# Optimization experiments

Hardware: AMD Instinct MI355X
Metric: run time of the kernel (lower is better)

## Reference

```python
import jax, jax.numpy as jnp
from jax import lax
import numpy as np

B, C, H, W = 4, 256, 64, 64
CQK = C // 8  # 32


def conv3x3(x, w, b):
    # x: [B,C_in,H,W], w: [C_out,C_in,3,3], b: [C_out]
    y = lax.conv_general_dilated(x, w, window_strides=(1, 1), padding='SAME',
                                 dimension_numbers=('NCHW', 'OIHW', 'NCHW'))
    return y + b[None, :, None, None]


def setup_inputs() -> dict:
    key = jax.random.key(0)
    ks = jax.random.split(key, 8)
    scale = 0.02
    return {
        'x': jax.random.normal(ks[0], (B, C, H, W), dtype=jnp.float32),
        'wq': jax.random.normal(ks[1], (CQK, C, 3, 3), dtype=jnp.float32) * scale,
        'bq': jax.random.normal(ks[2], (CQK,), dtype=jnp.float32) * scale,
        'wk': jax.random.normal(ks[3], (CQK, C, 3, 3), dtype=jnp.float32) * scale,
        'bk': jax.random.normal(ks[4], (CQK,), dtype=jnp.float32) * scale,
        'wv': jax.random.normal(ks[5], (C, C, 3, 3), dtype=jnp.float32) * scale,
        'bv': jax.random.normal(ks[6], (C,), dtype=jnp.float32) * scale,
        'gamma': jax.random.normal(ks[7], (1,), dtype=jnp.float32) * scale,
    }


def reference(x, wq, bq, wk, bk, wv, bv, gamma):
    b, c, h, w = x.shape
    n = h * w
    # Q: [B, N, C//8]  (permute(0,2,1) of the flattened conv output)
    q = conv3x3(x, wq, bq).reshape(b, -1, n).transpose(0, 2, 1)
    # K: [B, C//8, N]
    k = conv3x3(x, wk, bk).reshape(b, -1, n)
    # s: [B, N_q, N_k]
    s = jnp.einsum('bqd,bdk->bqk', q, k)
    # NOTE: original uses Softmax(dim=-2), i.e. over the QUERY axis
    attn_T = jax.nn.softmax(s, axis=-2)
    # V: [B, C, N]
    v = conv3x3(x, wv, bv).reshape(b, c, n)
    # o = bmm(V, attn_T): [B, C, N]
    o = jnp.einsum('bcq,bqk->bck', v, attn_T).reshape(b, c, h, w)
    return x + gamma * o
```

## Files before the change

### kernel.cpp

```cpp
#include <hip/hip_runtime.h>
#include <cstddef>

#define N_PIX 4096
#define HW 64
#define LOG2E 1.4426950408889634f
#define SHIFT2 28.8539008177793f

typedef __attribute__((ext_vector_type(8))) short bf16x8;
typedef __attribute__((ext_vector_type(4))) float f32x4;
typedef unsigned int u32;

static __device__ __forceinline__ unsigned short f2bf(float f) {
    union { float f; unsigned u; } v; v.f = f;
    unsigned r = v.u + 0x7fffu + ((v.u >> 16) & 1u);
    return (unsigned short)(r >> 16);
}
static __device__ __forceinline__ float bf2f(unsigned short s) {
    union { unsigned u; float f; } v; v.u = (unsigned)s << 16;
    return v.f;
}
static __device__ __forceinline__ unsigned pack_bf16_trunc(float lo, float hi) {
    union { float f; unsigned u; } a, b; a.f = hi; b.f = lo;
    return __builtin_amdgcn_perm(a.u, b.u, 0x07060302u);
}
static __device__ __forceinline__ void gll16(const void* g, void* l) {
    __builtin_amdgcn_global_load_lds(
        (const __attribute__((address_space(1))) u32*)g,
        (__attribute__((address_space(3))) u32*)l, 16, 0, 0);
}

__global__ __launch_bounds__(256) void prep_kernel(
    const float* __restrict__ x, unsigned short* __restrict__ xbf,
    const float* __restrict__ wq, const float* __restrict__ wk,
    const float* __restrict__ wv, unsigned short* __restrict__ wAll,
    unsigned short* __restrict__ zp)
{
    const int tid = threadIdx.x;
    if (blockIdx.z < 4) {
        __shared__ unsigned short Ts[64][72];
        const int px0 = blockIdx.x * 64, ci0 = blockIdx.y * 64, b = blockIdx.z;
        const float* xb = x + ((size_t)b * 256 + ci0) * N_PIX;

#pragma unroll
        for (int r = 0; r < 4; ++r) {
            int c = r * 16 + (tid >> 4);
            int p4 = (tid & 15) * 4;
            float4 v = *(const float4*)&xb[(size_t)c * N_PIX + px0 + p4];
            Ts[c][p4 + 0] = f2bf(v.x);
            Ts[c][p4 + 1] = f2bf(v.y);
            Ts[c][p4 + 2] = f2bf(v.z);
            Ts[c][p4 + 3] = f2bf(v.w);
        }
        __syncthreads();
#pragma unroll
        for (int r = 0; r < 2; ++r) {
            int id = tid * 2 + r;
            int p = id >> 3, c8 = (id & 7) * 8;
            ushort4 lo, hi;
            lo.x = Ts[c8 + 0][p]; lo.y = Ts[c8 + 1][p];
            lo.z = Ts[c8 + 2][p]; lo.w = Ts[c8 + 3][p];
            hi.x = Ts[c8 + 4][p]; hi.y = Ts[c8 + 5][p];
            hi.z = Ts[c8 + 6][p]; hi.w = Ts[c8 + 7][p];
            size_t off = ((size_t)b * N_PIX + px0 + p) * 256 + ci0 + c8;
            *(ushort4*)&xbf[off]     = lo;
            *(ushort4*)&xbf[off + 4] = hi;
        }
    } else {
        const int f = blockIdx.y * 64 + blockIdx.x;
#pragma unroll
        for (int base = 0; base < 2; ++base) {
            int gid = base * 65536 + f * 256 + tid;
            if (gid < 256) zp[gid] = 0;
            if (gid >= 72 * 320 * 4) continue;
            int part = gid & 3;
            int m = (gid >> 2) % 320;
            int kb = gid / 1280;
            int t = kb >> 3;
            int ci0 = (kb & 7) * 32 + part * 8;
            const float* src; int co; float sc = 1.f;
            if (m < 256)      { src = wv; co = m; }
            else if (m < 288) { src = wq; co = m - 256; sc = LOG2E; }
            else              { src = wk; co = m - 288; }
            ushort4 lo, hi;
            lo.x = f2bf(sc * src[((size_t)co * 256 + ci0 + 0) * 9 + t]);
            lo.y = f2bf(sc * src[((size_t)co * 256 + ci0 + 1) * 9 + t]);
            lo.z = f2bf(sc * src[((size_t)co * 256 + ci0 + 2) * 9 + t]);
            lo.w = f2bf(sc * src[((size_t)co * 256 + ci0 + 3) * 9 + t]);
            hi.x = f2bf(sc * src[((size_t)co * 256 + ci0 + 4) * 9 + t]);
            hi.y = f2bf(sc * src[((size_t)co * 256 + ci0 + 5) * 9 + t]);
            hi.z = f2bf(sc * src[((size_t)co * 256 + ci0 + 6) * 9 + t]);
            hi.w = f2bf(sc * src[((size_t)co * 256 + ci0 + 7) * 9 + t]);
            size_t off = ((size_t)kb * 320 + m) * 32 + part * 8;
            *(ushort4*)&wAll[off]     = lo;
            *(ushort4*)&wAll[off + 4] = hi;
        }
    }
}

__global__ __launch_bounds__(256, 2) void conv_gemm_v7(
    const unsigned short* __restrict__ xbf, const unsigned short* __restrict__ wAll,
    const float* __restrict__ bq, const float* __restrict__ bk,
    const float* __restrict__ bv, const unsigned short* __restrict__ zpage,
    unsigned short* __restrict__ vbf, unsigned short* __restrict__ qt,
    unsigned short* __restrict__ kt)
{
    __shared__ unsigned short Bl[4 * 7168];

    const int tid = threadIdx.x;
    const int w = tid >> 6, lane = tid & 63, quad = lane >> 4, l15 = lane & 15;
    const int y = blockIdx.x, rh = blockIdx.y, b = blockIdx.z;
    const int rg = w >> 1;
    const int pxh = w & 1;

    const unsigned short* xb = xbf + (size_t)b * N_PIX * 256;
    const unsigned short* aSrc = wAll + (size_t)rh * 160 * 32;

    auto stage = [&](int kb, int buf) {
        const int t_ = kb >> 3;
        const int ty = t_ / 3;
        const int dy = ty - 1, dx = t_ - ty * 3 - 1;
        const int gy = y + dy;
        const bool rowOK = ((unsigned)gy < 64u);
        const int ci0 = (kb & 7) * 32;
        const unsigned short* aS = aSrc + (size_t)kb * 10240;
        unsigned short* tile = &Bl[buf * 7168];
#pragma unroll
        for (int r = 0; r < 4; ++r) {
            const int c = r * 4 + w;
            if (r == 3 && w >= 2) continue;
            if (c < 10) {
                int o = c * 1024 + lane * 16;
                int u = o ^ (((o >> 7) & 7) << 4);
                gll16(aS + (u >> 1), tile + c * 512);
            } else {
                int o = (c - 10) * 1024 + lane * 16;
                int u = o ^ (((o >> 7) & 7) << 4);
                int px = u >> 6, k16 = (u >> 4) & 3;
                int gx = px + dx;
                const unsigned short* src =
                    (rowOK && (unsigned)gx < 64u)
                        ? xb + ((size_t)(gy * 64 + gx) * 256 + ci0 + k16 * 8)
                        : zpage;
                gll16(src, tile + 5120 + (c - 10) * 512);
            }
        }
    };

    f32x4 acc[5][2];
#pragma unroll
    for (int cb = 0; cb < 5; ++cb)
#pragma unroll
        for (int jb = 0; jb < 2; ++jb) acc[cb][jb] = (f32x4){0.f, 0.f, 0.f, 0.f};

    stage(0, 0);
    stage(1, 1);
    stage(2, 2);
    if (w < 2) asm volatile("s_waitcnt vmcnt(8)" ::: "memory");
    else       asm volatile("s_waitcnt vmcnt(6)" ::: "memory");
    __builtin_amdgcn_s_barrier();
    __builtin_amdgcn_sched_barrier(0);

    for (int kb = 0; kb < 72; ++kb) {
        const int buf = kb & 3;
        if (kb + 3 < 72) stage(kb + 3, (kb + 3) & 3);

        const int bb = buf * 7168;
        bf16x8 af[5], bfr[2];
#pragma unroll
        for (int cb = 0; cb < 5; ++cb) {
            int sr = rg * 80 + cb * 16 + l15;
            int u = sr * 64 + quad * 16;
            u ^= ((u >> 7) & 7) << 4;
            af[cb] = *(const bf16x8*)&Bl[bb + (u >> 1)];
        }
#pragma unroll
        for (int jb = 0; jb < 2; ++jb) {
            int px = pxh * 32 + jb * 16 + l15;
            int u = px * 64 + quad * 16;
            u ^= ((u >> 7) & 7) << 4;
            bfr[jb] = *(const bf16x8*)&Bl[bb + 5120 + (u >> 1)];
        }
        __builtin_amdgcn_s_setprio(1);
#pragma unroll
        for (int cb = 0; cb < 5; ++cb)
#pragma unroll
            for (int jb = 0; jb < 2; ++jb)
                acc[cb][jb] = __builtin_amdgcn_mfma_f32_16x16x32_bf16(
                    af[cb], bfr[jb], acc[cb][jb], 0, 0, 0);
        __builtin_amdgcn_s_setprio(0);

        if (kb + 3 < 72) {
            if (w < 2) asm volatile("s_waitcnt vmcnt(8)" ::: "memory");
            else       asm volatile("s_waitcnt vmcnt(6)" ::: "memory");
        } else if (kb + 2 < 72) {
            if (w < 2) asm volatile("s_waitcnt vmcnt(4)" ::: "memory");
            else       asm volatile("s_waitcnt vmcnt(3)" ::: "memory");
        } else if (kb + 1 < 72) {
            asm volatile("s_waitcnt vmcnt(0)" ::: "memory");
        }
        if (kb + 1 < 72) {
            __builtin_amdgcn_s_barrier();
            __builtin_amdgcn_sched_barrier(0);
        }
    }

#pragma unroll
    for (int cb = 0; cb < 5; ++cb) {
        int cBase = rh * 160 + rg * 80 + cb * 16 + quad * 4;
#pragma unroll
        for (int r = 0; r < 4; ++r) {
            int c = cBase + r;
            if (c < 256) {
                float bias = bv[c];
#pragma unroll
                for (int jb = 0; jb < 2; ++jb) {
                    int px = y * 64 + pxh * 32 + jb * 16 + l15;
                    vbf[((size_t)b * 256 + c) * N_PIX + px] = f2bf(acc[cb][jb][r] + bias);
                }
            } else if (c < 288) {
                float bias = bq[c - 256] * LOG2E;
#pragma unroll
                for (int jb = 0; jb < 2; ++jb) {
                    int px = y * 64 + pxh * 32 + jb * 16 + l15;
                    qt[((size_t)b * N_PIX + px) * 32 + (c - 256)] = f2bf(acc[cb][jb][r] + bias);
                }
            } else {
                float bias = bk[c - 288];
#pragma unroll
                for (int jb = 0; jb < 2; ++jb) {
                    int px = y * 64 + pxh * 32 + jb * 16 + l15;
                    kt[((size_t)b * N_PIX + px) * 32 + (c - 288)] = f2bf(acc[cb][jb][r] + bias);
                }
            }
        }
    }
}

__global__ __launch_bounds__(256, 2) void fused_attn_mfma(
    const unsigned short* __restrict__ qt, const unsigned short* __restrict__ kt,
    const unsigned short* __restrict__ vbf,
    unsigned short* __restrict__ Abuf, float* __restrict__ lbuf, int iRange)
{
    const int tid  = threadIdx.x;
    const int w    = tid >> 6;
    const int lane = tid & 63;
    const int quad = lane >> 4;
    const int l15  = lane & 15;
    const int j0   = blockIdx.x * 128;
    const int b    = blockIdx.y;
    const int sp   = blockIdx.z;
    const int iBeg = sp * iRange;
    const int NI   = iRange / 64;

    const unsigned short* qtb = qt + (size_t)b * N_PIX * 32;
    const unsigned short* ktb = kt + (size_t)b * N_PIX * 32;
    const unsigned short* vb  = vbf + (size_t)b * 256 * N_PIX;

    __shared__ unsigned Pfrag[2][4096];
    __shared__ float lred[4][128];

    bf16x8 kf[8];
#pragma unroll
    for (int jb = 0; jb < 8; ++jb)
        kf[jb] = *(const bf16x8*)&ktb[((size_t)(j0 + jb * 16 + l15)) * 32 + quad * 8];

    f32x4 acc[4][8];
#pragma unroll
    for (int cb = 0; cb < 4; ++cb)
#pragma unroll
        for (int jb = 0; jb < 8; ++jb)
            acc[cb][jb] = (f32x4){0.f, 0.f, 0.f, 0.f};

    float lpart[8] = {0.f, 0.f, 0.f, 0.f, 0.f, 0.f, 0.f, 0.f};

    const int wFrag = w >> 1;
    const int wL    = ((w & 1) << 5) + ((quad >> 1) << 4) + l15;
    const int wEl2  = (quad & 1) << 1;

    bf16x8 va[2][4];

    auto s_phase = [&](bf16x8 qa, int buf) {
#pragma unroll
        for (int jb = 0; jb < 8; ++jb) {
            f32x4 s = __builtin_amdgcn_mfma_f32_16x16x32_bf16(
                qa, kf[jb], (f32x4){-SHIFT2, -SHIFT2, -SHIFT2, -SHIFT2}, 0, 0, 0);
            float p0 = __builtin_amdgcn_exp2f(s[0]);
            float p1 = __builtin_amdgcn_exp2f(s[1]);
            float p2 = __builtin_amdgcn_exp2f(s[2]);
            float p3 = __builtin_amdgcn_exp2f(s[3]);
            lpart[jb] += (p0 + p1) + (p2 + p3);
            unsigned u0 = pack_bf16_trunc(p0, p1);
            unsigned u1 = pack_bf16_trunc(p2, p3);
            unsigned base = (((jb << 1) + wFrag) * 64 + wL) * 4 + wEl2;
            Pfrag[buf][base]     = u0;
            Pfrag[buf][base + 1] = u1;
        }
    };

    auto load_qa = [&](int i0) {
        return *(const bf16x8*)&qtb[((size_t)(i0 + w * 16 + l15)) * 32 + quad * 8];
    };
    auto load_va = [&](int i0) {
#pragma unroll
        for (int ks = 0; ks < 2; ++ks)
#pragma unroll
            for (int cb = 0; cb < 4; ++cb)
                va[ks][cb] = *(const bf16x8*)&vb[((size_t)(w * 64 + cb * 16 + l15)) * N_PIX
                                                 + i0 + ks * 32 + quad * 8];
    };

    load_va(iBeg);
    s_phase(load_qa(iBeg), 0);

    for (int n = 0; n < NI; ++n) {
        __syncthreads();
        const bool hasN = (n + 1 < NI);
        const int inext = iBeg + (n + 1) * 64;
        bf16x8 qaN;
        if (hasN) qaN = load_qa(inext);

#pragma unroll
        for (int ks = 0; ks < 2; ++ks) {
            bf16x8 pb[8];
#pragma unroll
            for (int jb = 0; jb < 8; ++jb)
                pb[jb] = *(const bf16x8*)&Pfrag[n & 1][(((jb << 1) + ks) * 64 + lane) * 4];
            __builtin_amdgcn_s_setprio(1);
#pragma unroll
            for (int cb = 0; cb < 4; ++cb)
#pragma unroll
                for (int jb = 0; jb < 8; ++jb)
                    acc[cb][jb] = __builtin_amdgcn_mfma_f32_16x16x32_bf16(
                        va[ks][cb], pb[jb], acc[cb][jb], 0, 0, 0);
            __builtin_amdgcn_s_setprio(0);
        }

        if (hasN) {
            load_va(inext);
            s_phase(qaN, (n + 1) & 1);
        }
    }

#pragma unroll
    for (int jb = 0; jb < 8; ++jb) {
        float v = lpart[jb];
        v += __shfl_xor(v, 16, 64);
        v += __shfl_xor(v, 32, 64);
        lpart[jb] = v;
    }
    if (lane < 16) {
#pragma unroll
        for (int jb = 0; jb < 8; ++jb)
            lred[w][jb * 16 + l15] = lpart[jb];
    }
    __syncthreads();
    if (tid < 128) {
        float s = lred[0][tid] + lred[1][tid] + lred[2][tid] + lred[3][tid];
        lbuf[((size_t)sp * 4 + b) * N_PIX + j0 + tid] = s;
    }

    unsigned short* Ab = Abuf + ((size_t)sp * 4 + b) * 256 * N_PIX;
#pragma unroll
    for (int cb = 0; cb < 4; ++cb) {
        int c = w * 64 + cb * 16 + quad * 4;
#pragma unroll
        for (int jb = 0; jb < 8; ++jb) {
            int j = j0 + jb * 16 + l15;
#pragma unroll
            for (int r = 0; r < 4; ++r)
                Ab[(size_t)(c + r) * N_PIX + j] = f2bf(acc[cb][jb][r]);
        }
    }
}

__global__ __launch_bounds__(256) void combine_kernel(
    const unsigned short* __restrict__ A, const float* __restrict__ L,
    const float* __restrict__ x, const float* __restrict__ gamma,
    float* __restrict__ out, int split)
{
    const size_t CH = (size_t)4 * 256 * N_PIX;
    size_t flat = ((size_t)blockIdx.x * 256 + threadIdx.x) * 8;
    int j = (int)(flat & (N_PIX - 1));
    int b = (int)(flat >> 20);

    float a[8] = {0.f, 0.f, 0.f, 0.f, 0.f, 0.f, 0.f, 0.f};
    float l[8] = {0.f, 0.f, 0.f, 0.f, 0.f, 0.f, 0.f, 0.f};
    for (int s = 0; s < split; ++s) {
        ushort4 av0 = *(const ushort4*)&A[flat + (size_t)s * CH];
        ushort4 av1 = *(const ushort4*)&A[flat + (size_t)s * CH + 4];
        a[0] += bf2f(av0.x); a[1] += bf2f(av0.y); a[2] += bf2f(av0.z); a[3] += bf2f(av0.w);
        a[4] += bf2f(av1.x); a[5] += bf2f(av1.y); a[6] += bf2f(av1.z); a[7] += bf2f(av1.w);
        float4 l0 = *(const float4*)&L[((size_t)s * 4 + b) * N_PIX + j];
        float4 l1 = *(const float4*)&L[((size_t)s * 4 + b) * N_PIX + j + 4];
        l[0] += l0.x; l[1] += l0.y; l[2] += l0.z; l[3] += l0.w;
        l[4] += l1.x; l[5] += l1.y; l[6] += l1.z; l[7] += l1.w;
    }
    float g = gamma[0];
    float4 x0 = *(const float4*)&x[flat];
    float4 x1 = *(const float4*)&x[flat + 4];
    float4 o0, o1;
    o0.x = x0.x + g * a[0] / l[0];
    o0.y = x0.y + g * a[1] / l[1];
    o0.z = x0.z + g * a[2] / l[2];
    o0.w = x0.w + g * a[3] / l[3];
    o1.x = x1.x + g * a[4] / l[4];
    o1.y = x1.y + g * a[5] / l[5];
    o1.z = x1.z + g * a[6] / l[6];
    o1.w = x1.w + g * a[7] / l[7];
    *(float4*)&out[flat]     = o0;
    *(float4*)&out[flat + 4] = o1;
}

extern "C" void kernel_launch(void* const* d_in, const int* in_sizes, int n_in,
                              void* d_out, int out_size, void* d_ws, size_t ws_size,
                              hipStream_t stream)
{
    const float* x     = (const float*)d_in[0];
    const float* wq    = (const float*)d_in[1];
    const float* bq    = (const float*)d_in[2];
    const float* wk    = (const float*)d_in[3];
    const float* bk    = (const float*)d_in[4];
    const float* wv    = (const float*)d_in[5];
    const float* bv    = (const float*)d_in[6];
    const float* gamma = (const float*)d_in[7];
    float* out = (float*)d_out;

    const size_t szQTel  = (size_t)4 * N_PIX * 32;
    const size_t szVBFel = (size_t)4 * 256 * N_PIX;
    const size_t szXBFel = (size_t)4 * N_PIX * 256;
    const size_t szWel   = (size_t)72 * 320 * 32;
    const size_t fixedB  = (2 * szQTel + szVBFel + szXBFel + szWel + 256) * 2;

    int split = 4;
    while (split > 1) {
        size_t need = fixedB
                    + (size_t)split * 4 * 256 * N_PIX * 2
                    + (size_t)split * 4 * N_PIX * 4;
        if (need <= ws_size) break;
        split >>= 1;
    }

    unsigned short* Abuf = (unsigned short*)d_ws;
    float* lbuf = (float*)(Abuf + (size_t)split * 4 * 256 * N_PIX);
    unsigned short* qt    = (unsigned short*)(lbuf + (size_t)split * 4 * N_PIX);
    unsigned short* kt    = qt + szQTel;
    unsigned short* vbf   = kt + szQTel;
    unsigned short* xbf   = vbf + szVBFel;
    unsigned short* wAll  = xbf + szXBFel;
    unsigned short* zpage = wAll + szWel;

    prep_kernel<<<dim3(N_PIX / 64, 4, 5), 256, 0, stream>>>(
        x, xbf, wq, wk, wv, wAll, zpage);

    conv_gemm_v7<<<dim3(HW, 2, 4), 256, 0, stream>>>(
        xbf, wAll, bq, bk, bv, zpage, vbf, qt, kt);

    fused_attn_mfma<<<dim3(N_PIX / 128, 4, split), 256, 0, stream>>>(
        qt, kt, vbf, Abuf, lbuf, N_PIX / split);

    combine_kernel<<<dim3((4 * 256 * N_PIX) / (256 * 8)), 256, 0, stream>>>(
        Abuf, lbuf, x, gamma, out, split);
}
```

Before: 179.2 us.

## Tile conv GEMM over two image rows and use triple buffering

```diff
diff --git a/kernel.cpp b/kernel.cpp
--- a/kernel.cpp
+++ b/kernel.cpp
@@ -97,20 +97,22 @@
     }
 }
 
-__global__ __launch_bounds__(256, 2) void conv_gemm_v7(
+__global__ __launch_bounds__(256, 2) void conv_gemm_v8(
     const unsigned short* __restrict__ xbf, const unsigned short* __restrict__ wAll,
     const float* __restrict__ bq, const float* __restrict__ bk,
     const float* __restrict__ bv, const unsigned short* __restrict__ zpage,
     unsigned short* __restrict__ vbf, unsigned short* __restrict__ qt,
     unsigned short* __restrict__ kt)
 {
-    __shared__ unsigned short Bl[4 * 7168];
+    __shared__ unsigned short Bl[3 * 9216];
 
     const int tid = threadIdx.x;
     const int w = tid >> 6, lane = tid & 63, quad = lane >> 4, l15 = lane & 15;
-    const int y = blockIdx.x, rh = blockIdx.y, b = blockIdx.z;
+    const int yt = blockIdx.x;
+    const int rh = blockIdx.y, b = blockIdx.z;
     const int rg = w >> 1;
     const int pxh = w & 1;
+    const int y0 = yt * 2;
 
     const unsigned short* xb = xbf + (size_t)b * N_PIX * 256;
     const unsigned short* aSrc = wAll + (size_t)rh * 160 * 32;
@@ -119,15 +121,13 @@
         const int t_ = kb >> 3;
         const int ty = t_ / 3;
         const int dy = ty - 1, dx = t_ - ty * 3 - 1;
-        const int gy = y + dy;
-        const bool rowOK = ((unsigned)gy < 64u);
         const int ci0 = (kb & 7) * 32;
         const unsigned short* aS = aSrc + (size_t)kb * 10240;
-        unsigned short* tile = &Bl[buf * 7168];
-#pragma unroll
-        for (int r = 0; r < 4; ++r) {
+        unsigned short* tile = &Bl[buf * 9216];
+#pragma unroll
+        for (int r = 0; r < 5; ++r) {
             const int c = r * 4 + w;
-            if (r == 3 && w >= 2) continue;
+            if (r == 4 && w >= 2) continue;
             if (c < 10) {
                 int o = c * 1024 + lane * 16;
                 int u = o ^ (((o >> 7) & 7) << 4);
@@ -135,10 +135,11 @@
             } else {
                 int o = (c - 10) * 1024 + lane * 16;
                 int u = o ^ (((o >> 7) & 7) << 4);
-                int px = u >> 6, k16 = (u >> 4) & 3;
-                int gx = px + dx;
+                int px = (u >> 6) & 127, k16 = (u >> 4) & 3;
+                int iy = px >> 6, ix = px & 63;
+                int gy = y0 + iy + dy, gx = ix + dx;
                 const unsigned short* src =
-                    (rowOK && (unsigned)gx < 64u)
+                    ((unsigned)gy < 64u && (unsigned)gx < 64u)
                         ? xb + ((size_t)(gy * 64 + gx) * 256 + ci0 + k16 * 8)
                         : zpage;
                 gll16(src, tile + 5120 + (c - 10) * 512);
@@ -146,26 +147,29 @@
         }
     };
 
-    f32x4 acc[5][2];
+    f32x4 acc[5][4];
 #pragma unroll
     for (int cb = 0; cb < 5; ++cb)
 #pragma unroll
-        for (int jb = 0; jb < 2; ++jb) acc[cb][jb] = (f32x4){0.f, 0.f, 0.f, 0.f};
+        for (int jb = 0; jb < 4; ++jb) acc[cb][jb] = (f32x4){0.f, 0.f, 0.f, 0.f};
 
     stage(0, 0);
     stage(1, 1);
-    stage(2, 2);
-    if (w < 2) asm volatile("s_waitcnt vmcnt(8)" ::: "memory");
-    else       asm volatile("s_waitcnt vmcnt(6)" ::: "memory");
+    if (w < 2) asm volatile("s_waitcnt vmcnt(5)" ::: "memory");
+    else       asm volatile("s_waitcnt vmcnt(4)" ::: "memory");
     __builtin_amdgcn_s_barrier();
     __builtin_amdgcn_sched_barrier(0);
 
+    int buf = 0;
     for (int kb = 0; kb < 72; ++kb) {
-        const int buf = kb & 3;
-        if (kb + 3 < 72) stage(kb + 3, (kb + 3) & 3);
-
-        const int bb = buf * 7168;
-        bf16x8 af[5], bfr[2];
+        int nb = buf + 1; if (nb == 3) nb = 0;
+        int pb = nb + 1;  if (pb == 3) pb = 0;
+        const bool more2 = (kb + 2 < 72);
+        const bool more1 = (kb + 1 < 72);
+        if (more2) stage(kb + 2, pb);
+
+        const int bb = buf * 9216;
+        bf16x8 af[5], bfr[4];
 #pragma unroll
         for (int cb = 0; cb < 5; ++cb) {
             int sr = rg * 80 + cb * 16 + l15;
@@ -174,8 +178,8 @@
             af[cb] = *(const bf16x8*)&Bl[bb + (u >> 1)];
         }
 #pragma unroll
-        for (int jb = 0; jb < 2; ++jb) {
-            int px = pxh * 32 + jb * 16 + l15;
+        for (int jb = 0; jb < 4; ++jb) {
+            int px = pxh * 64 + jb * 16 + l15;
             int u = px * 64 + quad * 16;
             u ^= ((u >> 7) & 7) << 4;
             bfr[jb] = *(const bf16x8*)&Bl[bb + 5120 + (u >> 1)];
@@ -184,24 +188,22 @@
 #pragma unroll
         for (int cb = 0; cb < 5; ++cb)
 #pragma unroll
-            for (int jb = 0; jb < 2; ++jb)
+            for (int jb = 0; jb < 4; ++jb)
                 acc[cb][jb] = __builtin_amdgcn_mfma_f32_16x16x32_bf16(
                     af[cb], bfr[jb], acc[cb][jb], 0, 0, 0);
         __builtin_amdgcn_s_setprio(0);
 
-        if (kb + 3 < 72) {
-            if (w < 2) asm volatile("s_waitcnt vmcnt(8)" ::: "memory");
-            else       asm volatile("s_waitcnt vmcnt(6)" ::: "memory");
-        } else if (kb + 2 < 72) {
-            if (w < 2) asm volatile("s_waitcnt vmcnt(4)" ::: "memory");
-            else       asm volatile("s_waitcnt vmcnt(3)" ::: "memory");
-        } else if (kb + 1 < 72) {
+        if (more2) {
+            if (w < 2) asm volatile("s_waitcnt vmcnt(5)" ::: "memory");
+            else       asm volatile("s_waitcnt vmcnt(4)" ::: "memory");
+        } else if (more1) {
             asm volatile("s_waitcnt vmcnt(0)" ::: "memory");
         }
-        if (kb + 1 < 72) {
+        if (more1) {
             __builtin_amdgcn_s_barrier();
             __builtin_amdgcn_sched_barrier(0);
         }
+        buf = nb;
     }
 
 #pragma unroll
@@ -213,22 +215,22 @@
             if (c < 256) {
                 float bias = bv[c];
 #pragma unroll
-                for (int jb = 0; jb < 2; ++jb) {
-                    int px = y * 64 + pxh * 32 + jb * 16 + l15;
+                for (int jb = 0; jb < 4; ++jb) {
+                    int px = yt * 128 + pxh * 64 + jb * 16 + l15;
                     vbf[((size_t)b * 256 + c) * N_PIX + px] = f2bf(acc[cb][jb][r] + bias);
                 }
             } else if (c < 288) {
                 float bias = bq[c - 256] * LOG2E;
 #pragma unroll
-                for (int jb = 0; jb < 2; ++jb) {
-                    int px = y * 64 + pxh * 32 + jb * 16 + l15;
+                for (int jb = 0; jb < 4; ++jb) {
+                    int px = yt * 128 + pxh * 64 + jb * 16 + l15;
                     qt[((size_t)b * N_PIX + px) * 32 + (c - 256)] = f2bf(acc[cb][jb][r] + bias);
                 }
             } else {
                 float bias = bk[c - 288];
 #pragma unroll
-                for (int jb = 0; jb < 2; ++jb) {
-                    int px = y * 64 + pxh * 32 + jb * 16 + l15;
+                for (int jb = 0; jb < 4; ++jb) {
+                    int px = yt * 128 + pxh * 64 + jb * 16 + l15;
                     kt[((size_t)b * N_PIX + px) * 32 + (c - 288)] = f2bf(acc[cb][jb][r] + bias);
                 }
             }
@@ -325,14 +327,12 @@
 #pragma unroll
             for (int jb = 0; jb < 8; ++jb)
                 pb[jb] = *(const bf16x8*)&Pfrag[n & 1][(((jb << 1) + ks) * 64 + lane) * 4];
-            __builtin_amdgcn_s_setprio(1);
 #pragma unroll
             for (int cb = 0; cb < 4; ++cb)
 #pragma unroll
                 for (int jb = 0; jb < 8; ++jb)
                     acc[cb][jb] = __builtin_amdgcn_mfma_f32_16x16x32_bf16(
                         va[ks][cb], pb[jb], acc[cb][jb], 0, 0, 0);
-            __builtin_amdgcn_s_setprio(0);
         }
 
         if (hasN) {
@@ -452,7 +452,7 @@
     prep_kernel<<<dim3(N_PIX / 64, 4, 5), 256, 0, stream>>>(
         x, xbf, wq, wk, wv, wAll, zpage);
 
-    conv_gemm_v7<<<dim3(HW, 2, 4), 256, 0, stream>>>(
+    conv_gemm_v8<<<dim3(32, 2, 4), 256, 0, stream>>>(
         xbf, wAll, bq, bk, bv, zpage, vbf, qt, kt);
 
     fused_attn_mfma<<<dim3(N_PIX / 128, 4, split), 256, 0, stream>>>(
```

After: 186.1 us. 1.04x slower.
